# Optimization experiments

Hardware: AMD Instinct MI355X
Metric: run time of the kernel (lower is better)

Reference implementation:

```python
import jax, jax.numpy as jnp
import numpy as np

B, C, H, W = 4, 512, 32, 32
NUM_HEADS, DIM_HEAD = 16, 32
DIM_ATTN = NUM_HEADS * DIM_HEAD  # 512
N = H * W


def setup_inputs() -> dict:
    key = jax.random.key(0)
    ks = jax.random.split(key, 6)
    s = 0.02
    return {
        "x": jax.random.normal(ks[0], (B, C, H, W), jnp.float32),
        "w_qkv": jax.random.normal(ks[1], (3 * DIM_ATTN, C), jnp.float32) * s,
        "b_qkv": jax.random.normal(ks[2], (3 * DIM_ATTN,), jnp.float32) * s,
        "w_proj": jax.random.normal(ks[3], (C, DIM_ATTN), jnp.float32) * s,
        "b_proj": jax.random.normal(ks[4], (C,), jnp.float32) * s,
        "shared_rel_pos": jax.random.normal(ks[5], (1, NUM_HEADS, N, N), jnp.float32) * s,
    }


def reference(x, w_qkv, b_qkv, w_proj, b_proj, shared_rel_pos):
    b, c, h, w = x.shape
    n = h * w
    scale = DIM_HEAD ** -0.5
    # 1x1 conv == per-pixel matmul over channels
    qkv = jnp.einsum('bchw,oc->bohw', x, w_qkv) + b_qkv[None, :, None, None]
    # [B, heads, 3*dh, N] -> chunk along dim 2 (matches torch .chunk(3, dim=2))
    qkv = qkv.reshape(b, NUM_HEADS, 3 * DIM_HEAD, n)
    q, k, v = jnp.split(qkv, 3, axis=2)          # each [B, heads, dh, N]
    attn = jnp.einsum('bhdi,bhdj->bhij', q, k) * scale  # q^T @ k
    attn = attn + shared_rel_pos
    attn = jax.nn.softmax(attn, axis=-1)
    out = jnp.einsum('bhdj,bhij->bhdi', v, attn)  # v @ attn^T, [B, heads, dh, N]
    out = out.reshape(b, NUM_HEADS * DIM_HEAD, h, w)
    out = jnp.einsum('bchw,oc->bohw', out, w_proj) + b_proj[None, :, None, None]
    return out
```

## Files before the change

### kernel.cpp

```cpp
#include <hip/hip_runtime.h>
#include <cstdint>
#include <cstddef>

#define BATCH 4
#define CIN   512
#define NPIX  1024
#define HEADS 16
#define DH    32
#define DATTN 512
#define O_QKV 1536

typedef unsigned short u16;
typedef __bf16 bf16x8 __attribute__((ext_vector_type(8)));
typedef float  f32x4  __attribute__((ext_vector_type(4)));

typedef const __attribute__((address_space(1))) void g1_t;
typedef __attribute__((address_space(3))) void l3_t;

__device__ __forceinline__ u16 f2bf(float f) {
  unsigned u = __float_as_uint(f);
  u += 0x7fffu + ((u >> 16) & 1u);
  return (u16)(u >> 16);
}

__device__ __forceinline__ void gl_lds16(const void* gp, void* lp) {
  __builtin_amdgcn_global_load_lds((g1_t*)gp, (l3_t*)lp, 16, 0, 0);
}

__global__ __launch_bounds__(256) void prep_w(const float* __restrict__ w1,
                                              const float* __restrict__ w2,
                                              u16* __restrict__ o1,
                                              u16* __restrict__ o2) {
  const int idx = blockIdx.x * 256 + threadIdx.x;
  const int n1 = (O_QKV * CIN) >> 2;
  float4 v = (idx < n1) ? reinterpret_cast<const float4*>(w1)[idx]
                        : reinterpret_cast<const float4*>(w2)[idx - n1];
  uint2 pk = make_uint2((unsigned)f2bf(v.x) | ((unsigned)f2bf(v.y) << 16),
                        (unsigned)f2bf(v.z) | ((unsigned)f2bf(v.w) << 16));
  if (idx < n1) reinterpret_cast<uint2*>(o1)[idx] = pk;
  else          reinterpret_cast<uint2*>(o2)[idx - n1] = pk;
}

__global__ __launch_bounds__(256) void prep_x(const float* __restrict__ x,
                                              u16* __restrict__ xt) {
  __shared__ float sT[64][65];
  const int t  = threadIdx.x;
  const int n0 = blockIdx.x * 64;
  const int c0 = blockIdx.y * 64;
  const int b  = blockIdx.z;
  const float* xb = x + ((size_t)b * CIN + c0) * NPIX + n0;
#pragma unroll
  for (int i = 0; i < 4; ++i) {
    int r   = i * 16 + (t >> 4);
    int col = (t & 15) << 2;
    float4 v = *reinterpret_cast<const float4*>(&xb[(size_t)r * NPIX + col]);
    sT[r][col + 0] = v.x; sT[r][col + 1] = v.y;
    sT[r][col + 2] = v.z; sT[r][col + 3] = v.w;
  }
  __syncthreads();
#pragma unroll
  for (int i = 0; i < 2; ++i) {
    int nl = t >> 2;
    int ch = (t & 3) + (i << 2);
    u16 tmp[8];
#pragma unroll
    for (int e = 0; e < 8; ++e) tmp[e] = f2bf(sT[(ch << 3) + e][nl]);
    *reinterpret_cast<uint4*>(&xt[((size_t)b * NPIX + n0 + nl) * CIN + c0 + (ch << 3)]) =
        *reinterpret_cast<uint4*>(tmp);
  }
}

__global__ __launch_bounds__(256) void gemm_qkv_mfma(const u16* __restrict__ wq,
                                                     const u16* __restrict__ xt,
                                                     const float* __restrict__ bias,
                                                     u16* __restrict__ qt,
                                                     u16* __restrict__ kt,
                                                     u16* __restrict__ vt) {
  __shared__ __align__(16) u16 sA[96 * 64];
  __shared__ __align__(16) u16 sB[128 * 64];
  const int t  = threadIdx.x;
  const int w  = t >> 6, l = t & 63, g = l >> 4, ln = l & 15;
  const int n0 = blockIdx.x * 128;
  const int h  = blockIdx.y;
  const int b  = blockIdx.z;
  const int wm = w >> 1, wn = w & 1;

  const u16* wbase = wq + (size_t)h * 96 * CIN;
  const u16* xbase = xt + ((size_t)b * NPIX + n0) * CIN;

  f32x4 acc[3][4];
#pragma unroll
  for (int mi = 0; mi < 3; ++mi)
#pragma unroll
    for (int ni = 0; ni < 4; ++ni) acc[mi][ni] = {0.f, 0.f, 0.f, 0.f};

  for (int k0 = 0; k0 < CIN; k0 += 64) {
#pragma unroll
    for (int i = 0; i < 3; ++i) {
      int chunk = i * 256 + (w << 6) + l;
      gl_lds16(wbase + ((size_t)(chunk >> 3)) * CIN + k0 + ((chunk & 7) << 3),
               (char*)sA + i * 4096 + (w << 10));
    }
#pragma unroll
    for (int i = 0; i < 4; ++i) {
      int chunk = i * 256 + (w << 6) + l;
      gl_lds16(xbase + ((size_t)(chunk >> 3)) * CIN + k0 + ((chunk & 7) << 3),
               (char*)sB + i * 4096 + (w << 10));
    }
    __syncthreads();
#pragma unroll
    for (int kk = 0; kk < 64; kk += 32) {
      bf16x8 af[3], bfr[4];
#pragma unroll
      for (int mi = 0; mi < 3; ++mi)
        af[mi] = *reinterpret_cast<const bf16x8*>(&sA[(48 * wm + 16 * mi + ln) * 64 + kk + (g << 3)]);
#pragma unroll
      for (int ni = 0; ni < 4; ++ni)
        bfr[ni] = *reinterpret_cast<const bf16x8*>(&sB[((wn << 6) + (ni << 4) + ln) * 64 + kk + (g << 3)]);
#pragma unroll
      for (int mi = 0; mi < 3; ++mi)
#pragma unroll
        for (int ni = 0; ni < 4; ++ni)
          acc[mi][ni] = __builtin_amdgcn_mfma_f32_16x16x32_bf16(af[mi], bfr[ni], acc[mi][ni], 0, 0, 0);
    }
    __syncthreads();
  }

  const float* bh = bias + h * 96;
#pragma unroll
  for (int mi = 0; mi < 3; ++mi) {
    const int sec = 48 * wm + 16 * mi;
    const int rb  = sec + (g << 2);
    const float b0 = bh[rb + 0], b1 = bh[rb + 1], b2 = bh[rb + 2], b3 = bh[rb + 3];
#pragma unroll
    for (int ni = 0; ni < 4; ++ni) {
      const int n = n0 + (wn << 6) + (ni << 4) + ln;
      f32x4 a = acc[mi][ni];
      u16 e0 = f2bf(a[0] + b0), e1 = f2bf(a[1] + b1);
      u16 e2 = f2bf(a[2] + b2), e3 = f2bf(a[3] + b3);
      if (sec < 32) {
        const int d = sec + (g << 2);
        uint2 pk = make_uint2((unsigned)e0 | ((unsigned)e1 << 16),
                              (unsigned)e2 | ((unsigned)e3 << 16));
        *reinterpret_cast<uint2*>(&qt[(((size_t)(b * HEADS + h)) * NPIX + n) * DH + d]) = pk;
      } else if (sec < 64) {
        const int d = sec - 32 + (g << 2);
        uint2 pk = make_uint2((unsigned)e0 | ((unsigned)e1 << 16),
                              (unsigned)e2 | ((unsigned)e3 << 16));
        *reinterpret_cast<uint2*>(&kt[(((size_t)(b * HEADS + h)) * NPIX + n) * DH + d]) = pk;
      } else {
        const int d = sec - 64 + (g << 2);
        u16* vp = &vt[(((size_t)(b * HEADS + h)) * DH + d) * NPIX + n];
        vp[0] = e0; vp[NPIX] = e1; vp[2 * NPIX] = e2; vp[3 * NPIX] = e3;
      }
    }
  }
}

__global__ __launch_bounds__(512, 4) void attn_mfma(const u16* __restrict__ qt,
                                                    const u16* __restrict__ kt,
                                                    const u16* __restrict__ vt,
                                                    const float* __restrict__ rel,
                                                    u16* __restrict__ aout) {
  __shared__ __align__(16) u16 sK[2][2 * 2048];
  __shared__ __align__(16) u16 sV[2][2 * 2048];
  __shared__ __align__(16) u16 sP[8][16 * 72];

  const int t  = threadIdx.x;
  const int w  = t >> 6, l = t & 63, g = l >> 4, ln = l & 15;
  const int bid = blockIdx.x;
  const int xcd = bid & 7, sl = bid >> 3;
  const int h   = (xcd << 1) | (sl >> 5);
  const int i0  = ((sl >> 1) & 15) << 6;
  const int bp  = sl & 1;
  const int bw  = (bp << 1) | (w >> 2);
  const int iw  = w & 3;
  const float scale = 0.17677669529663687f;

  bf16x8 qf = *reinterpret_cast<const bf16x8*>(
      qt + (((size_t)(bw * HEADS + h)) * NPIX + i0 + (iw << 4) + ln) * DH + (g << 3));

  f32x4 vzero = {0.f, 0.f, 0.f, 0.f};
  f32x4 accO[2] = {vzero, vzero};
  float l_lane[4] = {0.f, 0.f, 0.f, 0.f};

  {
  }
  const int sc_b  = (bp << 1) | (t >> 8);
  const int sc_cb = t & 255;
  const int sc_r  = sc_cb >> 3;
  const int sc_cl = (sc_cb & 7) ^ (sc_r & 7);
  const u16* ksrc0 = kt + (((size_t)(sc_b * HEADS + h)) * NPIX +
                           ((sc_r << 1) | (sc_cl >> 2))) * DH + ((sc_cl & 3) << 3);
  const u16* vsrc0 = vt + (((size_t)(sc_b * HEADS + h)) * DH + sc_r) * NPIX + (sc_cl << 3);

#define STAGE(js_, p_) do {                                               \
    gl_lds16(ksrc0 + (size_t)(js_) * 2048, (char*)&sK[p_][0] + (w << 10)); \
    gl_lds16(vsrc0 + (size_t)(js_) * 64,   (char*)&sV[p_][0] + (w << 10)); \
  } while (0)

  const float* relp = rel + ((size_t)h * NPIX + i0 + (iw << 4) + (g << 2)) * NPIX + ln;
  float relA[16], relB[16];
#pragma unroll
  for (int jj = 0; jj < 4; ++jj)
#pragma unroll
    for (int v = 0; v < 4; ++v)
      relA[(jj << 2) + v] = relp[(size_t)v * NPIX + (jj << 4)];

  STAGE(0, 0);

  u16* sPw = &sP[w][0];
  const int lb = w >> 2;

  for (int js = 0; js < 16; ++js) {
    const int p = js & 1;
    __syncthreads();
    if (js < 15) {
      STAGE(js + 1, p ^ 1);
#pragma unroll
      for (int jj = 0; jj < 4; ++jj)
#pragma unroll
        for (int v = 0; v < 4; ++v)
          relB[(jj << 2) + v] = relp[(size_t)v * NPIX + ((js + 1) << 6) + (jj << 4)];
    }

    const u16* Kb = &sK[p][lb << 11];
    const u16* Vb = &sV[p][lb << 11];

    f32x4 sfr[4];
#pragma unroll
    for (int jj = 0; jj < 4; ++jj) {
      const int r  = (jj << 3) + (ln >> 1);
      const int ks = (((ln & 1) << 2) | g) ^ ((ln >> 1) & 7);
      bf16x8 kf = *reinterpret_cast<const bf16x8*>(Kb + r * 64 + ks * 8);
      sfr[jj] = __builtin_amdgcn_mfma_f32_16x16x32_bf16(qf, kf, vzero, 0, 0, 0);
    }

#pragma unroll
    for (int v = 0; v < 4; ++v) {
      float p0 = __expf(sfr[0][v] * scale + relA[0 + v]);
      float p1 = __expf(sfr[1][v] * scale + relA[4 + v]);
      float p2 = __expf(sfr[2][v] * scale + relA[8 + v]);
      float p3 = __expf(sfr[3][v] * scale + relA[12 + v]);
      l_lane[v] += (p0 + p1) + (p2 + p3);
      const int prow = ((g << 2) + v) * 72 + ln;
      sPw[prow +  0] = f2bf(p0);
      sPw[prow + 16] = f2bf(p1);
      sPw[prow + 32] = f2bf(p2);
      sPw[prow + 48] = f2bf(p3);
    }

#pragma unroll
    for (int kc = 0; kc < 2; ++kc) {
      bf16x8 pa = *reinterpret_cast<const bf16x8*>(sPw + ln * 72 + (kc << 5) + (g << 3));
#pragma unroll
      for (int dc = 0; dc < 2; ++dc) {
        const int d  = (dc << 4) + ln;
        const int vs = ((kc << 2) | g) ^ (d & 7);
        bf16x8 vf = *reinterpret_cast<const bf16x8*>(Vb + d * 64 + vs * 8);
        accO[dc] = __builtin_amdgcn_mfma_f32_16x16x32_bf16(pa, vf, accO[dc], 0, 0, 0);
      }
    }

    if (js < 15) {
#pragma unroll
      for (int e = 0; e < 16; ++e) relA[e] = relB[e];
    }
  }
#undef STAGE

#pragma unroll
  for (int v = 0; v < 4; ++v) {
    float ls = l_lane[v];
    ls += __shfl_xor(ls, 1);
    ls += __shfl_xor(ls, 2);
    ls += __shfl_xor(ls, 4);
    ls += __shfl_xor(ls, 8);
    const float inv = 1.f / ls;
    const size_t row = (size_t)bw * NPIX + i0 + (iw << 4) + (g << 2) + v;
    aout[row * DATTN + (h << 5) + ln]      = f2bf(accO[0][v] * inv);
    aout[row * DATTN + (h << 5) + 16 + ln] = f2bf(accO[1][v] * inv);
  }
}

__global__ __launch_bounds__(256) void gemm_proj_mfma(const u16* __restrict__ wp,
                                                      const u16* __restrict__ at,
                                                      const float* __restrict__ bias,
                                                      float* __restrict__ out) {
  __shared__ __align__(16) u16 sA[64 * 64];
  __shared__ __align__(16) u16 sB[128 * 64];
  const int t  = threadIdx.x;
  const int w  = t >> 6, l = t & 63, g = l >> 4, ln = l & 15;
  const int n0 = blockIdx.x * 128;
  const int o0 = blockIdx.y * 64;
  const int b  = blockIdx.z;
  const int wm = w >> 1, wn = w & 1;

  const u16* wbase = wp + (size_t)o0 * DATTN;
  const u16* abase = at + ((size_t)b * NPIX + n0) * DATTN;

  f32x4 acc[2][4];
#pragma unroll
  for (int mi = 0; mi < 2; ++mi)
#pragma unroll
    for (int ni = 0; ni < 4; ++ni) acc[mi][ni] = {0.f, 0.f, 0.f, 0.f};

  for (int k0 = 0; k0 < DATTN; k0 += 64) {
#pragma unroll
    for (int i = 0; i < 2; ++i) {
      int chunk = i * 256 + (w << 6) + l;
      gl_lds16(wbase + ((size_t)(chunk >> 3)) * DATTN + k0 + ((chunk & 7) << 3),
               (char*)sA + i * 4096 + (w << 10));
    }
#pragma unroll
    for (int i = 0; i < 4; ++i) {
      int chunk = i * 256 + (w << 6) + l;
      gl_lds16(abase + ((size_t)(chunk >> 3)) * DATTN + k0 + ((chunk & 7) << 3),
               (char*)sB + i * 4096 + (w << 10));
    }
    __syncthreads();
#pragma unroll
    for (int kk = 0; kk < 64; kk += 32) {
      bf16x8 af[2], bfr[4];
#pragma unroll
      for (int mi = 0; mi < 2; ++mi)
        af[mi] = *reinterpret_cast<const bf16x8*>(&sA[((wm << 5) + (mi << 4) + ln) * 64 + kk + (g << 3)]);
#pragma unroll
      for (int ni = 0; ni < 4; ++ni)
        bfr[ni] = *reinterpret_cast<const bf16x8*>(&sB[((wn << 6) + (ni << 4) + ln) * 64 + kk + (g << 3)]);
#pragma unroll
      for (int mi = 0; mi < 2; ++mi)
#pragma unroll
        for (int ni = 0; ni < 4; ++ni)
          acc[mi][ni] = __builtin_amdgcn_mfma_f32_16x16x32_bf16(af[mi], bfr[ni], acc[mi][ni], 0, 0, 0);
    }
    __syncthreads();
  }

#pragma unroll
  for (int mi = 0; mi < 2; ++mi) {
    const int o = o0 + (wm << 5) + (mi << 4) + (g << 2);
    const float b0 = bias[o], b1 = bias[o + 1], b2 = bias[o + 2], b3 = bias[o + 3];
#pragma unroll
    for (int ni = 0; ni < 4; ++ni) {
      const int n = n0 + (wn << 6) + (ni << 4) + ln;
      float* op = &out[((size_t)b * DATTN + o) * NPIX + n];
      op[0]        = acc[mi][ni][0] + b0;
      op[NPIX]     = acc[mi][ni][1] + b1;
      op[2 * NPIX] = acc[mi][ni][2] + b2;
      op[3 * NPIX] = acc[mi][ni][3] + b3;
    }
  }
}

extern "C" void kernel_launch(void* const* d_in, const int* in_sizes, int n_in,
                              void* d_out, int out_size, void* d_ws, size_t ws_size,
                              hipStream_t stream) {
  (void)in_sizes; (void)n_in; (void)out_size; (void)ws_size;
  const float* x      = (const float*)d_in[0];
  const float* w_qkv  = (const float*)d_in[1];
  const float* b_qkv  = (const float*)d_in[2];
  const float* w_proj = (const float*)d_in[3];
  const float* b_proj = (const float*)d_in[4];
  const float* rel    = (const float*)d_in[5];
  float* out = (float*)d_out;

  u16* xt    = (u16*)d_ws;
  u16* wq_bf = xt + (size_t)BATCH * NPIX * CIN;
  u16* wp_bf = wq_bf + (size_t)O_QKV * CIN;
  u16* qt    = wp_bf + (size_t)DATTN * DATTN;
  u16* kt    = qt + (size_t)BATCH * HEADS * NPIX * DH;
  u16* vt    = kt + (size_t)BATCH * HEADS * NPIX * DH;
  u16* aout  = vt + (size_t)BATCH * HEADS * NPIX * DH;

  prep_w<<<1024, 256, 0, stream>>>(w_qkv, w_proj, wq_bf, wp_bf);
  prep_x<<<dim3(NPIX / 64, CIN / 64, BATCH), 256, 0, stream>>>(x, xt);
  gemm_qkv_mfma<<<dim3(NPIX / 128, HEADS, BATCH), 256, 0, stream>>>(wq_bf, xt, b_qkv, qt, kt, vt);
  attn_mfma<<<512, 512, 0, stream>>>(qt, kt, vt, rel, aout);
  gemm_proj_mfma<<<dim3(NPIX / 128, DATTN / 64, BATCH), 256, 0, stream>>>(wp_bf, aout, b_proj, out);
}
```

Measured before the change: 70.98 us.

## Vectorize rel-pos loads, fold softmax scale into Q, use exp2 and packed P stores

Remaps the key columns each lane owns so that every lane handles 4 contiguous j positions. This lets the relative-position bias be fetched as float4 loads instead of 16 scalar strided loads, and lets P be written to LDS as one packed 4xbf16 store per row with a new padding and XOR swizzle. The attention scale and log2(e) are folded into Q in the QKV epilogue, so softmax becomes a single fma plus a hardware exp2. The risks are extra bf16 rounding from storing pre-scaled Q and possible LDS bank conflicts from the new swizzle.

```diff
diff --git a/kernel.cpp b/kernel.cpp
--- a/kernel.cpp
+++ b/kernel.cpp
@@ -9,13 +9,24 @@
 #define DH    32
 #define DATTN 512
 #define O_QKV 1536
+#define PPAD  88
 
 typedef unsigned short u16;
+typedef __bf16 bf16x4 __attribute__((ext_vector_type(4)));
 typedef __bf16 bf16x8 __attribute__((ext_vector_type(8)));
 typedef float  f32x4  __attribute__((ext_vector_type(4)));
 
 typedef const __attribute__((address_space(1))) void g1_t;
 typedef __attribute__((address_space(3))) void l3_t;
+
+#if defined(__has_builtin)
+#if __has_builtin(__builtin_amdgcn_exp2f)
+#define EXP2(x) __builtin_amdgcn_exp2f(x)
+#endif
+#endif
+#ifndef EXP2
+#define EXP2(x) __expf((x) * 0.6931471805599453f)
+#endif
 
 __device__ __forceinline__ u16 f2bf(float f) {
   unsigned u = __float_as_uint(f);
@@ -126,6 +137,7 @@
     __syncthreads();
   }
 
+  const float QSC = 0.17677669529663687f * 1.4426950408889634f;
   const float* bh = bias + h * 96;
 #pragma unroll
   for (int mi = 0; mi < 3; ++mi) {
@@ -136,8 +148,9 @@
     for (int ni = 0; ni < 4; ++ni) {
       const int n = n0 + (wn << 6) + (ni << 4) + ln;
       f32x4 a = acc[mi][ni];
-      u16 e0 = f2bf(a[0] + b0), e1 = f2bf(a[1] + b1);
-      u16 e2 = f2bf(a[2] + b2), e3 = f2bf(a[3] + b3);
+      float v0 = a[0] + b0, v1 = a[1] + b1, v2 = a[2] + b2, v3 = a[3] + b3;
+      if (sec < 32) { v0 *= QSC; v1 *= QSC; v2 *= QSC; v3 *= QSC; }
+      u16 e0 = f2bf(v0), e1 = f2bf(v1), e2 = f2bf(v2), e3 = f2bf(v3);
       if (sec < 32) {
         const int d = sec + (g << 2);
         uint2 pk = make_uint2((unsigned)e0 | ((unsigned)e1 << 16),
@@ -164,7 +177,7 @@
                                                     u16* __restrict__ aout) {
   __shared__ __align__(16) u16 sK[2][2 * 2048];
   __shared__ __align__(16) u16 sV[2][2 * 2048];
-  __shared__ __align__(16) u16 sP[8][16 * 72];
+  __shared__ __align__(16) u16 sP[8][16 * PPAD];
 
   const int t  = threadIdx.x;
   const int w  = t >> 6, l = t & 63, g = l >> 4, ln = l & 15;
@@ -175,7 +188,7 @@
   const int bp  = sl & 1;
   const int bw  = (bp << 1) | (w >> 2);
   const int iw  = w & 3;
-  const float scale = 0.17677669529663687f;
+  const float LOG2E = 1.4426950408889634f;
 
   bf16x8 qf = *reinterpret_cast<const bf16x8*>(
       qt + (((size_t)(bw * HEADS + h)) * NPIX + i0 + (iw << 4) + ln) * DH + (g << 3));
@@ -184,28 +197,25 @@
   f32x4 accO[2] = {vzero, vzero};
   float l_lane[4] = {0.f, 0.f, 0.f, 0.f};
 
-  {
-  }
   const int sc_b  = (bp << 1) | (t >> 8);
   const int sc_cb = t & 255;
   const int sc_r  = sc_cb >> 3;
-  const int sc_cl = (sc_cb & 7) ^ (sc_r & 7);
+  const int sc_kc = (sc_cb & 7) ^ (sc_r & 7) ^ ((sc_r >> 3) & 1);
+  const int sc_vc = (sc_cb & 7) ^ (sc_r & 7);
   const u16* ksrc0 = kt + (((size_t)(sc_b * HEADS + h)) * NPIX +
-                           ((sc_r << 1) | (sc_cl >> 2))) * DH + ((sc_cl & 3) << 3);
-  const u16* vsrc0 = vt + (((size_t)(sc_b * HEADS + h)) * DH + sc_r) * NPIX + (sc_cl << 3);
+                           ((sc_r << 1) | (sc_kc >> 2))) * DH + ((sc_kc & 3) << 3);
+  const u16* vsrc0 = vt + (((size_t)(sc_b * HEADS + h)) * DH + sc_r) * NPIX + (sc_vc << 3);
 
 #define STAGE(js_, p_) do {                                               \
     gl_lds16(ksrc0 + (size_t)(js_) * 2048, (char*)&sK[p_][0] + (w << 10)); \
     gl_lds16(vsrc0 + (size_t)(js_) * 64,   (char*)&sV[p_][0] + (w << 10)); \
   } while (0)
 
-  const float* relp = rel + ((size_t)h * NPIX + i0 + (iw << 4) + (g << 2)) * NPIX + ln;
-  float relA[16], relB[16];
-#pragma unroll
-  for (int jj = 0; jj < 4; ++jj)
-#pragma unroll
-    for (int v = 0; v < 4; ++v)
-      relA[(jj << 2) + v] = relp[(size_t)v * NPIX + (jj << 4)];
+  const float* relp = rel + ((size_t)h * NPIX + i0 + (iw << 4) + (g << 2)) * NPIX + (ln << 2);
+  f32x4 relA4[4], relB4[4];
+#pragma unroll
+  for (int v = 0; v < 4; ++v)
+    relA4[v] = *reinterpret_cast<const f32x4*>(relp + (size_t)v * NPIX);
 
   STAGE(0, 0);
 
@@ -218,10 +228,8 @@
     if (js < 15) {
       STAGE(js + 1, p ^ 1);
 #pragma unroll
-      for (int jj = 0; jj < 4; ++jj)
-#pragma unroll
-        for (int v = 0; v < 4; ++v)
-          relB[(jj << 2) + v] = relp[(size_t)v * NPIX + ((js + 1) << 6) + (jj << 4)];
+      for (int v = 0; v < 4; ++v)
+        relB4[v] = *reinterpret_cast<const f32x4*>(relp + (size_t)v * NPIX + ((js + 1) << 6));
     }
 
     const u16* Kb = &sK[p][lb << 11];
@@ -230,29 +238,27 @@
     f32x4 sfr[4];
 #pragma unroll
     for (int jj = 0; jj < 4; ++jj) {
-      const int r  = (jj << 3) + (ln >> 1);
-      const int ks = (((ln & 1) << 2) | g) ^ ((ln >> 1) & 7);
+      const int r  = (ln << 1) + (jj >> 1);
+      const int ks = ((((jj & 1) << 2) | g) ^ (r & 7)) ^ ((r >> 3) & 1);
       bf16x8 kf = *reinterpret_cast<const bf16x8*>(Kb + r * 64 + ks * 8);
       sfr[jj] = __builtin_amdgcn_mfma_f32_16x16x32_bf16(qf, kf, vzero, 0, 0, 0);
     }
 
 #pragma unroll
     for (int v = 0; v < 4; ++v) {
-      float p0 = __expf(sfr[0][v] * scale + relA[0 + v]);
-      float p1 = __expf(sfr[1][v] * scale + relA[4 + v]);
-      float p2 = __expf(sfr[2][v] * scale + relA[8 + v]);
-      float p3 = __expf(sfr[3][v] * scale + relA[12 + v]);
+      float p0 = EXP2(fmaf(relA4[v][0], LOG2E, sfr[0][v]));
+      float p1 = EXP2(fmaf(relA4[v][1], LOG2E, sfr[1][v]));
+      float p2 = EXP2(fmaf(relA4[v][2], LOG2E, sfr[2][v]));
+      float p3 = EXP2(fmaf(relA4[v][3], LOG2E, sfr[3][v]));
       l_lane[v] += (p0 + p1) + (p2 + p3);
-      const int prow = ((g << 2) + v) * 72 + ln;
-      sPw[prow +  0] = f2bf(p0);
-      sPw[prow + 16] = f2bf(p1);
-      sPw[prow + 32] = f2bf(p2);
-      sPw[prow + 48] = f2bf(p3);
+      bf16x4 pk;
+      pk[0] = (__bf16)p0; pk[1] = (__bf16)p1; pk[2] = (__bf16)p2; pk[3] = (__bf16)p3;
+      *reinterpret_cast<bf16x4*>(sPw + ((g << 2) + v) * PPAD + (ln << 2)) = pk;
     }
 
 #pragma unroll
     for (int kc = 0; kc < 2; ++kc) {
-      bf16x8 pa = *reinterpret_cast<const bf16x8*>(sPw + ln * 72 + (kc << 5) + (g << 3));
+      bf16x8 pa = *reinterpret_cast<const bf16x8*>(sPw + ln * PPAD + (kc << 5) + (g << 3));
 #pragma unroll
       for (int dc = 0; dc < 2; ++dc) {
         const int d  = (dc << 4) + ln;
@@ -264,7 +270,7 @@
 
     if (js < 15) {
 #pragma unroll
-      for (int e = 0; e < 16; ++e) relA[e] = relB[e];
+      for (int v = 0; v < 4; ++v) relA4[v] = relB4[v];
     }
   }
 #undef STAGE
```

Measured after the change: 66.18 us. 6.8% less time.
